# Kernel optimization log

Measured on AMD Instinct MI355X. Metric: run time of the kernel, lower is better.

The kernel has to match this reference:

```python
import jax, jax.numpy as jnp
import numpy as np

N, E, B = 4096, 12288, 64
CLIP, HID, H = 768, 1024, 4
PREFIX, MBART = 4, 768
C2 = PREFIX * MBART
NEG_SLOPE = 0.2


def setup_inputs() -> dict:
    key = jax.random.key(0)
    ks = jax.random.split(key, 30)
    s = 0.05

    def nrm(k, shape, sc=s):
        return jax.random.normal(k, shape, dtype=jnp.float32) * sc

    inp = {
        "x": nrm(ks[0], (N, CLIP), 1.0),
        "edge_index": jax.random.randint(ks[1], (2, E), 0, N),
        "edge_attr": nrm(ks[2], (E, CLIP), 1.0),
        "batch": jnp.sort(jax.random.randint(ks[3], (N,), 0, B)),
        # GATConv 1 (clip_dim -> hidden, H heads, concat=False)
        "W1": nrm(ks[4], (CLIP, H, HID)),
        "att_src1": nrm(ks[5], (H, HID)),
        "att_dst1": nrm(ks[6], (H, HID)),
        "W_edge1": nrm(ks[7], (CLIP, H, HID)),
        "att_edge1": nrm(ks[8], (H, HID)),
        "bias1": jnp.zeros((HID,), jnp.float32),
        "prelu1": jnp.float32(0.25),
        # GATConv 2 (hidden -> prefix*mbart, H heads, concat=False)
        "W2": nrm(ks[9], (HID, H, C2)),
        "att_src2": nrm(ks[10], (H, C2)),
        "att_dst2": nrm(ks[11], (H, C2)),
        "W_edge2": nrm(ks[12], (CLIP, H, C2)),
        "att_edge2": nrm(ks[13], (H, C2)),
        "bias2": jnp.zeros((C2,), jnp.float32),
        "prelu2": jnp.float32(0.25),
        # AttentionalAggregation gate_nn: Linear/PReLU/Linear/PReLU/Linear
        "gW1": nrm(ks[14], (C2, HID)),
        "gb1": jnp.zeros((HID,), jnp.float32),
        "ga1": jnp.float32(0.25),
        "gW2": nrm(ks[15], (HID, HID)),
        "gb2": jnp.zeros((HID,), jnp.float32),
        "ga2": jnp.float32(0.25),
        "gW3": nrm(ks[16], (HID, 1)),
        "gb3": jnp.zeros((1,), jnp.float32),
    }
    return inp


def _prelu(x, a):
    return jnp.where(x >= 0, x, a * x)


def _gat_conv(x, src, dst, edge_attr, W, att_s, att_d, W_e, att_e, bias, n):
    # PyG GATConv, concat=False: shared lin for src/dst, edge-attention term,
    # leaky_relu, segment softmax over destination neighborhoods, scatter-add.
    xl = jnp.einsum('nd,dhc->nhc', x, W)                  # [N,H,C]
    a_s = jnp.einsum('nhc,hc->nh', xl, att_s)             # [N,H]
    a_d = jnp.einsum('nhc,hc->nh', xl, att_d)             # [N,H]
    # fuse lin_edge + att_edge: alpha_e = edge_attr @ (W_e . att_e)
    w_e = jnp.einsum('dhc,hc->dh', W_e, att_e)            # [D_edge,H]
    a_e = edge_attr @ w_e                                 # [E,H]
    alpha = jax.nn.leaky_relu(a_s[src] + a_d[dst] + a_e, NEG_SLOPE)
    # segment softmax grouped by dst
    amax = jax.ops.segment_max(alpha, dst, num_segments=n)
    amax = jnp.where(jnp.isfinite(amax), amax, 0.0)
    ex = jnp.exp(alpha - amax[dst])
    den = jax.ops.segment_sum(ex, dst, num_segments=n)
    coef = ex / (den[dst] + 1e-16)                        # [E,H]
    msg = coef[:, :, None] * xl[src]                      # [E,H,C]
    out = jax.ops.segment_sum(msg, dst, num_segments=n)   # [N,H,C]
    return out.mean(axis=1) + bias                        # concat=False -> head mean


def _forward(x, edge_index, edge_attr, batch,
             W1, att_src1, att_dst1, W_edge1, att_edge1, bias1, prelu1,
             W2, att_src2, att_dst2, W_edge2, att_edge2, bias2, prelu2,
             gW1, gb1, ga1, gW2, gb2, ga2, gW3, gb3):
    n = x.shape[0]
    src, dst = edge_index[0], edge_index[1]
    # add_self_loops with fill_value='mean': self-loop edge_attr = mean of
    # incoming edge_attr per destination node (0 if isolated)
    ones = jnp.ones((src.shape[0],), x.dtype)
    deg = jax.ops.segment_sum(ones, dst, num_segments=n)
    mean_attr = jax.ops.segment_sum(edge_attr, dst, num_segments=n) / jnp.clip(deg, 1.0)[:, None]
    loops = jnp.arange(n)
    src_a = jnp.concatenate([src, loops])
    dst_a = jnp.concatenate([dst, loops])
    ea = jnp.concatenate([edge_attr, mean_attr], axis=0)

    h = _gat_conv(x, src_a, dst_a, ea, W1, att_src1, att_dst1, W_edge1, att_edge1, bias1, n)
    h = _prelu(h, prelu1)
    h = _gat_conv(h, src_a, dst_a, ea, W2, att_src2, att_dst2, W_edge2, att_edge2, bias2, n)
    h = _prelu(h, prelu2)

    # AttentionalAggregation: gate_nn -> segment softmax over batch -> weighted sum
    g = _prelu(h @ gW1 + gb1, ga1)
    g = _prelu(g @ gW2 + gb2, ga2)
    gate = g @ gW3 + gb3                                   # [N,1]
    gmax = jax.ops.segment_max(gate, batch, num_segments=B)
    gmax = jnp.where(jnp.isfinite(gmax), gmax, 0.0)
    eg = jnp.exp(gate - gmax[batch])
    den = jax.ops.segment_sum(eg, batch, num_segments=B)
    coef = eg / (den[batch] + 1e-16)
    pooled = jax.ops.segment_sum(coef * h, batch, num_segments=B)  # [B,C2]
    return pooled.reshape(-1, PREFIX, MBART)


def reference(x, edge_index, edge_attr, batch,
              W1, att_src1, att_dst1, W_edge1, att_edge1, bias1, prelu1,
              W2, att_src2, att_dst2, W_edge2, att_edge2, bias2, prelu2,
              gW1, gb1, ga1, gW2, gb2, ga2, gW3, gb3):
    return _forward(x, edge_index, edge_attr, batch,
                    W1, att_src1, att_dst1, W_edge1, att_edge1, bias1, prelu1,
                    W2, att_src2, att_dst2, W_edge2, att_edge2, bias2, prelu2,
                    gW1, gb1, ga1, gW2, gb2, ga2, gW3, gb3)
```

## Files before the change

### kernel.cpp

```cpp
#include <hip/hip_runtime.h>
#include <stdint.h>
#include <stddef.h>

#define N_NODES  4096
#define N_EDGES  12288
#define EA_EDGES 16384
#define NBATCH   64
#define CLIPD    768
#define HIDD     1024
#define C2D      3072
#define NEG_SLOPE 0.2f
#define MAXDEG   96

typedef unsigned short u16;
typedef short bf16x8 __attribute__((ext_vector_type(8)));
typedef float f32x4  __attribute__((ext_vector_type(4)));

static __device__ __forceinline__ float b2f(u16 u) {
    union { float f; unsigned int i; } v; v.i = ((unsigned int)u) << 16; return v.f;
}
static __device__ __forceinline__ u16 f2b(float f) {
    union { float f; unsigned int i; } v; v.f = f;
    unsigned int r = (v.i + 0x7fffu + ((v.i >> 16) & 1u)) >> 16;
    return (u16)r;
}
static __device__ __forceinline__ void ld4(const float* p, float v[4]) {
    float4 t = *(const float4*)p;
    v[0] = t.x; v[1] = t.y; v[2] = t.z; v[3] = t.w;
}
static __device__ __forceinline__ void ld4(const u16* p, float v[4]) {
    ushort4 t = *(const ushort4*)p;
    v[0] = b2f(t.x); v[1] = b2f(t.y); v[2] = b2f(t.z); v[3] = b2f(t.w);
}

static __device__ __forceinline__ float wsum(float v) {
#pragma unroll
    for (int o = 32; o > 0; o >>= 1) v += __shfl_xor(v, o, 64);
    return v;
}
static __device__ __forceinline__ float wmax(float v) {
#pragma unroll
    for (int o = 32; o > 0; o >>= 1) v = fmaxf(v, __shfl_xor(v, o, 64));
    return v;
}
static __device__ __forceinline__ int lower_bound(const int* a, int n, int key) {
    int lo = 0, hi = n;
    while (lo < hi) { int m = (lo + hi) >> 1; if (a[m] < key) lo = m + 1; else hi = m; }
    return lo;
}

#define GLD16(gp, lp)                                                            \
    __builtin_amdgcn_global_load_lds((const __attribute__((address_space(1))) void*)(gp), \
                                     (__attribute__((address_space(3))) void*)(lp), 16, 0, 0)

__global__ void k_deg(const int* __restrict__ dst, int* __restrict__ deg) {
    int e = blockIdx.x * 256 + threadIdx.x;
    if (e < N_EDGES) atomicAdd(&deg[dst[e]], 1);
}

__global__ void k_scan(const int* __restrict__ deg, int* __restrict__ offs) {
    __shared__ int s[1024];
    int t = threadIdx.x;
    int v[4]; int sum = 0;
#pragma unroll
    for (int i = 0; i < 4; i++) { v[i] = deg[t * 4 + i] + 1; sum += v[i]; }
    s[t] = sum; __syncthreads();
    for (int st = 1; st < 1024; st <<= 1) {
        int x = 0;
        if (t >= st) x = s[t - st];
        __syncthreads();
        s[t] += x;
        __syncthreads();
    }
    int run = s[t] - sum;
#pragma unroll
    for (int i = 0; i < 4; i++) { offs[t * 4 + i] = run; run += v[i]; }
    if (t == 1023) offs[N_NODES] = run;
}

__global__ void k_fill(const int* __restrict__ dst, const int* __restrict__ offs,
                       int* __restrict__ cur, int* __restrict__ csr) {
    int id = blockIdx.x * 256 + threadIdx.x;
    if (id >= EA_EDGES) return;
    int d = (id < N_EDGES) ? dst[id] : (id - N_EDGES);
    int p = atomicAdd(&cur[d], 1);
    csr[offs[d] + p] = id;
}

static __device__ void reduce_w_body(const float* __restrict__ W, const float* __restrict__ attA,
                                     const float* __restrict__ attB, float* __restrict__ out,
                                     int C, int col0, int d) {
    int t = threadIdx.x;
    float acc[8] = {0, 0, 0, 0, 0, 0, 0, 0};
    for (int c = t * 4; c < C; c += 1024) {
#pragma unroll
        for (int h = 0; h < 4; h++) {
            float4 w = *(const float4*)&W[((size_t)d * 4 + h) * C + c];
            float4 a = *(const float4*)&attA[h * C + c];
            acc[h] += w.x * a.x + w.y * a.y + w.z * a.z + w.w * a.w;
            if (attB) {
                float4 bv = *(const float4*)&attB[h * C + c];
                acc[4 + h] += w.x * bv.x + w.y * bv.y + w.z * bv.z + w.w * bv.w;
            }
        }
    }
    __shared__ float red[4][8];
    int lane = t & 63, wv = t >> 6;
#pragma unroll
    for (int j = 0; j < 8; j++) acc[j] = wsum(acc[j]);
    if (lane == 0) {
#pragma unroll
        for (int j = 0; j < 8; j++) red[wv][j] = acc[j];
    }
    __syncthreads();
    if (t < 8) {
        float s = red[0][t] + red[1][t] + red[2][t] + red[3][t];
        if (attB) out[d * 8 + col0 + t] = s;
        else if (t < 4) out[d * 8 + col0 + t] = s;
    }
}

__global__ void k_reduce_all(const float* __restrict__ W1, const float* __restrict__ as1,
                             const float* __restrict__ ad1, float* __restrict__ vsd1,
                             const float* __restrict__ We1, const float* __restrict__ ae1,
                             const float* __restrict__ W2, const float* __restrict__ as2,
                             const float* __restrict__ ad2, float* __restrict__ vsd2,
                             const float* __restrict__ We2, const float* __restrict__ ae2,
                             float* __restrict__ we12) {
    int b = blockIdx.x;
    if (b < CLIPD)                   reduce_w_body(W1, as1, ad1, vsd1, HIDD, 0, b);
    else if (b < 2 * CLIPD)          reduce_w_body(We1, ae1, nullptr, we12, HIDD, 0, b - CLIPD);
    else if (b < 2 * CLIPD + HIDD)   reduce_w_body(W2, as2, ad2, vsd2, C2D, 0, b - 2 * CLIPD);
    else                             reduce_w_body(We2, ae2, nullptr, we12, C2D, 4, b - 2 * CLIPD - HIDD);
}

template <typename T>
static __device__ void gemv8_body(const T* __restrict__ X, int K, const float* __restrict__ Wr,
                                  float* __restrict__ out, int row) {
    int lane = threadIdx.x & 63;
    float acc[8] = {0, 0, 0, 0, 0, 0, 0, 0};
    const T* xp = X + (size_t)row * K;
    for (int k = lane * 4; k < K; k += 256) {
        float xv[4]; ld4(xp + k, xv);
#pragma unroll
        for (int kk = 0; kk < 4; kk++) {
            const float4* w = (const float4*)(Wr + (size_t)(k + kk) * 8);
            float4 w0 = w[0], w1 = w[1];
            acc[0] += xv[kk] * w0.x; acc[1] += xv[kk] * w0.y;
            acc[2] += xv[kk] * w0.z; acc[3] += xv[kk] * w0.w;
            acc[4] += xv[kk] * w1.x; acc[5] += xv[kk] * w1.y;
            acc[6] += xv[kk] * w1.z; acc[7] += xv[kk] * w1.w;
        }
    }
#pragma unroll
    for (int j = 0; j < 8; j++) acc[j] = wsum(acc[j]);
    if (lane == 0) {
#pragma unroll
        for (int j = 0; j < 8; j++) out[(size_t)row * 8 + j] = acc[j];
    }
}

template <typename T>
__global__ void k_gemv8(const T* __restrict__ X, int K, const float* __restrict__ Wr,
                        float* __restrict__ out, int rows) {
    int row = blockIdx.x * 4 + (threadIdx.x >> 6);
    if (row < rows) gemv8_body(X, K, Wr, out, row);
}

__global__ void k_gemv8_dual(const float* __restrict__ Xa, const float* __restrict__ Wa,
                             float* __restrict__ outA, int rowsA,
                             const float* __restrict__ Xb, const float* __restrict__ Wb,
                             float* __restrict__ outB) {
    int row = blockIdx.x * 4 + (threadIdx.x >> 6);
    if (row < rowsA) gemv8_body(Xa, CLIPD, Wa, outA, row);
    else             gemv8_body(Xb, CLIPD, Wb, outB, row - rowsA);
}

__global__ void k_selfloop(float* __restrict__ ae, const int* __restrict__ csr,
                           const int* __restrict__ offs, const int* __restrict__ deg) {
    int n = blockIdx.x * 256 + threadIdx.x;
    if (n >= N_NODES) return;
    float s[8] = {0, 0, 0, 0, 0, 0, 0, 0};
    int lo = offs[n], hi = offs[n + 1];
    for (int i = lo; i < hi; i++) {
        int eid = csr[i];
        if (eid < N_EDGES) {
            const float4* p = (const float4*)(ae + (size_t)eid * 8);
            float4 a = p[0], b = p[1];
            s[0] += a.x; s[1] += a.y; s[2] += a.z; s[3] += a.w;
            s[4] += b.x; s[5] += b.y; s[6] += b.z; s[7] += b.w;
        }
    }
    float inv = 1.0f / (float)(deg[n] > 0 ? deg[n] : 1);
    float4* o = (float4*)(ae + (size_t)(N_EDGES + n) * 8);
    float4 o0, o1;
    o0.x = s[0] * inv; o0.y = s[1] * inv; o0.z = s[2] * inv; o0.w = s[3] * inv;
    o1.x = s[4] * inv; o1.y = s[5] * inv; o1.z = s[6] * inv; o1.w = s[7] * inv;
    o[0] = o0; o[1] = o1;
}

template <typename T>
__global__ void k_attn_agg(const T* __restrict__ feat, int D,
                           const float* __restrict__ asd, const float* __restrict__ ae, int aecol,
                           const int* __restrict__ offs, const int* __restrict__ csr,
                           const int* __restrict__ src, u16* __restrict__ agg) {
    int n = blockIdx.x, t = threadIdx.x;
    __shared__ int sl[MAXDEG];
    __shared__ float cf[MAXDEG][4];
    int lo = offs[n];
    int cnt = offs[n + 1] - lo;
    if (cnt > MAXDEG) cnt = MAXDEG;
    for (int i = t; i < cnt; i += 256) {
        int eid = csr[lo + i];
        int s = (eid < N_EDGES) ? src[eid] : n;
        sl[i] = s;
#pragma unroll
        for (int h = 0; h < 4; h++) {
            float al = asd[(size_t)s * 8 + h] + asd[(size_t)n * 8 + 4 + h] +
                       ae[(size_t)eid * 8 + aecol + h];
            cf[i][h] = (al >= 0.f) ? al : NEG_SLOPE * al;
        }
    }
    __syncthreads();
    {
        int wv = t >> 6, lane = t & 63;
        float mx = -1e30f;
        for (int i = lane; i < cnt; i += 64) mx = fmaxf(mx, cf[i][wv]);
        mx = wmax(mx);
        float ds = 0.f;
        for (int i = lane; i < cnt; i += 64) {
            float e = __expf(cf[i][wv] - mx); cf[i][wv] = e; ds += e;
        }
        ds = wsum(ds);
        float inv = 1.0f / (ds + 1e-16f);
        for (int i = lane; i < cnt; i += 64) cf[i][wv] *= inv;
    }
    __syncthreads();
    for (int d4 = t * 4; d4 < D; d4 += 1024) {
        float a[4][4] = {};
        for (int i = 0; i < cnt; i++) {
            float4 c4 = *(const float4*)cf[i];
            float v[4]; ld4(feat + (size_t)sl[i] * D + d4, v);
#pragma unroll
            for (int dj = 0; dj < 4; dj++) {
                a[dj][0] += c4.x * v[dj]; a[dj][1] += c4.y * v[dj];
                a[dj][2] += c4.z * v[dj]; a[dj][3] += c4.w * v[dj];
            }
        }
        u16* op = agg + (size_t)n * 4 * D + (size_t)d4 * 4;
#pragma unroll
        for (int dj = 0; dj < 4; dj++) {
            ushort4 pk;
            pk.x = f2b(a[dj][0]); pk.y = f2b(a[dj][1]);
            pk.z = f2b(a[dj][2]); pk.w = f2b(a[dj][3]);
            *(ushort4*)(op + dj * 4) = pk;
        }
    }
}

__global__ void k_transpose(const float* __restrict__ in, u16* __restrict__ out, int R, int C) {
    __shared__ float tile[64][65];
    int tx = threadIdx.x, ty = threadIdx.y;
    int rb = blockIdx.y * 64, cb = blockIdx.x * 64;
    for (int i = ty; i < 64; i += 4) tile[i][tx] = in[(size_t)(rb + i) * C + cb + tx];
    __syncthreads();
    int linear = ty * 64 + tx;
#pragma unroll
    for (int jj = 0; jj < 4; jj++) {
        int idx = linear + jj * 256;
        int j = idx >> 4, s4 = (idx & 15) * 4;
        ushort4 pk;
        pk.x = f2b(tile[s4 + 0][j]);
        pk.y = f2b(tile[s4 + 1][j]);
        pk.z = f2b(tile[s4 + 2][j]);
        pk.w = f2b(tile[s4 + 3][j]);
        *(ushort4*)(out + (size_t)(cb + j) * R + rb + s4) = pk;
    }
}

template <int BN, int KSUB>
__global__ __launch_bounds__(256, 2) void k_gemm(
        const u16* __restrict__ A, const u16* __restrict__ Bt, void* __restrict__ Cout,
        const float* __restrict__ bias, const float* __restrict__ prelu, float scale,
        int N, int K, int f32out) {
    constexpr int NJ = BN / 32;
    constexpr int NBCH = BN * 8 / 256;
    __shared__ __align__(16) u16 As[KSUB * 128 * 64];
    __shared__ __align__(16) u16 Bs[KSUB * BN * 64];
    int tid = threadIdx.x;
    int lane = tid & 63, wv = tid >> 6;
    int gx = gridDim.x;
    int bx = blockIdx.x, by = blockIdx.y;
    if ((gx & 7) == 0) {
        int flat = by * gx + bx;
        int nx_per = gx >> 3;
        int xcd = flat & 7, idx = flat >> 3;
        bx = xcd * nx_per + idx % nx_per;
        by = idx / nx_per;
    }
    int m0 = by * 128, n0 = bx * BN;
    const u16* agp[4]; int alo[4];
#pragma unroll
    for (int u = 0; u < 4; u++) {
        int c = tid + u * 256;
        int r = c >> 3, kb = (c & 7) ^ (r & 7);
        agp[u] = A + (size_t)(m0 + r) * K + kb * 8;
        alo[u] = c * 8;
    }
    const u16* bgp[NBCH]; int blo[NBCH];
#pragma unroll
    for (int u = 0; u < NBCH; u++) {
        int c = tid + u * 256;
        int r = c >> 3, kb = (c & 7) ^ (r & 7);
        bgp[u] = Bt + (size_t)(n0 + r) * K + kb * 8;
        blo[u] = c * 8;
    }
    int wm = wv & 1, wn = wv >> 1;
    int rl = lane & 15, q = lane >> 4;
    int swz = rl & 7;
    int mb = wm * 64 + rl;
    int nb = wn * (NJ * 16) + rl;
    f32x4 acc[4][NJ] = {};
    for (int k0 = 0; k0 < K; k0 += 64 * KSUB) {
        __syncthreads();
#pragma unroll
        for (int su = 0; su < KSUB; su++) {
#pragma unroll
            for (int u = 0; u < 4; u++)    GLD16(agp[u] + su * 64, As + su * (128 * 64) + alo[u]);
#pragma unroll
            for (int u = 0; u < NBCH; u++) GLD16(bgp[u] + su * 64, Bs + su * (BN * 64) + blo[u]);
        }
#pragma unroll
        for (int u = 0; u < 4; u++)    agp[u] += 64 * KSUB;
#pragma unroll
        for (int u = 0; u < NBCH; u++) bgp[u] += 64 * KSUB;
        __syncthreads();
#pragma unroll
        for (int su = 0; su < KSUB; su++) {
            const u16* Asb = As + su * (128 * 64);
            const u16* Bsb = Bs + su * (BN * 64);
            bf16x8 af[4][2], bfr[NJ][2];
#pragma unroll
            for (int i = 0; i < 4; i++)
#pragma unroll
                for (int s = 0; s < 2; s++)
                    af[i][s] = *(const bf16x8*)(Asb + (((mb + i * 16) * 8 + ((q + 4 * s) ^ swz)) * 8));
#pragma unroll
            for (int j = 0; j < NJ; j++)
#pragma unroll
                for (int s = 0; s < 2; s++)
                    bfr[j][s] = *(const bf16x8*)(Bsb + (((nb + j * 16) * 8 + ((q + 4 * s) ^ swz)) * 8));
#pragma unroll
            for (int i = 0; i < 4; i++)
#pragma unroll
                for (int j = 0; j < NJ; j++) {
                    acc[i][j] = __builtin_amdgcn_mfma_f32_16x16x32_bf16(af[i][0], bfr[j][0], acc[i][j], 0, 0, 0);
                    acc[i][j] = __builtin_amdgcn_mfma_f32_16x16x32_bf16(af[i][1], bfr[j][1], acc[i][j], 0, 0, 0);
                }
        }
    }
    float pa = prelu[0];
    int r0w = (lane >> 4) * 4;
    int cc = lane & 15;
#pragma unroll
    for (int j = 0; j < NJ; j++) {
        int col = n0 + wn * (NJ * 16) + j * 16 + cc;
        float bv = bias[col];
#pragma unroll
        for (int i = 0; i < 4; i++) {
#pragma unroll
            for (int r = 0; r < 4; r++) {
                int row = m0 + wm * 64 + i * 16 + r0w + r;
                float v = acc[i][j][r] * scale + bv;
                v = (v >= 0.f) ? v : pa * v;
                if (f32out) ((float*)Cout)[(size_t)row * N + col] = v;
                else        ((u16*)Cout)[(size_t)row * N + col] = f2b(v);
            }
        }
    }
}

__global__ void k_gate(const float* __restrict__ g2, const float* __restrict__ gW3,
                       const float* __restrict__ gb3, float* __restrict__ gate) {
    int wv = threadIdx.x >> 6, lane = threadIdx.x & 63;
    int n = blockIdx.x * 4 + wv;
    if (n >= N_NODES) return;
    float s = 0.f;
    const float* gp = g2 + (size_t)n * HIDD;
    for (int k = lane * 4; k < HIDD; k += 256) {
        float4 a = *(const float4*)(gp + k);
        float4 w = *(const float4*)(gW3 + k);
        s += a.x * w.x + a.y * w.y + a.z * w.z + a.w * w.w;
    }
    s = wsum(s);
    if (lane == 0) gate[n] = s + gb3[0];
}

__global__ void k_pool(const float* __restrict__ gate, const u16* __restrict__ h2,
                       const int* __restrict__ batch, float* __restrict__ out) {
    int b = blockIdx.x, t = threadIdx.x;
    int c = blockIdx.y * 1024 + t * 4;
    int lo = lower_bound(batch, N_NODES, b);
    int hi = lower_bound(batch, N_NODES, b + 1);
    int cnt = hi - lo;
    if (cnt <= 0) {
        float4 z; z.x = z.y = z.z = z.w = 0.f;
        *(float4*)(out + (size_t)b * C2D + c) = z;
        return;
    }
    if (cnt > 256) cnt = 256;
    __shared__ float w[256];
    __shared__ float red[4];
    int lane = t & 63, wv = t >> 6;
    float mx = -1e30f;
    for (int i = t; i < cnt; i += 256) mx = fmaxf(mx, gate[lo + i]);
    mx = wmax(mx);
    if (lane == 0) red[wv] = mx;
    __syncthreads();
    mx = fmaxf(fmaxf(red[0], red[1]), fmaxf(red[2], red[3]));
    __syncthreads();
    float ds = 0.f;
    for (int i = t; i < cnt; i += 256) { float e = __expf(gate[lo + i] - mx); w[i] = e; ds += e; }
    ds = wsum(ds);
    if (lane == 0) red[wv] = ds;
    __syncthreads();
    float inv = 1.0f / (red[0] + red[1] + red[2] + red[3] + 1e-16f);
    float4 acc; acc.x = acc.y = acc.z = acc.w = 0.f;
    const u16* hp = h2 + (size_t)lo * C2D + c;
    for (int i = 0; i < cnt; i++) {
        ushort4 hv = *(const ushort4*)hp; hp += C2D;
        float wi = w[i];
        acc.x += wi * b2f(hv.x); acc.y += wi * b2f(hv.y);
        acc.z += wi * b2f(hv.z); acc.w += wi * b2f(hv.w);
    }
    acc.x *= inv; acc.y *= inv; acc.z *= inv; acc.w *= inv;
    *(float4*)(out + (size_t)b * C2D + c) = acc;
}

extern "C" void kernel_launch(void* const* d_in, const int* in_sizes, int n_in,
                              void* d_out, int out_size, void* d_ws, size_t ws_size,
                              hipStream_t stream) {
    (void)in_sizes; (void)n_in; (void)out_size; (void)ws_size;
    const float* x      = (const float*)d_in[0];
    const int*   eidx   = (const int*)d_in[1];
    const float* eattr  = (const float*)d_in[2];
    const int*   batch  = (const int*)d_in[3];
    const float* W1     = (const float*)d_in[4];
    const float* att_s1 = (const float*)d_in[5];
    const float* att_d1 = (const float*)d_in[6];
    const float* We1    = (const float*)d_in[7];
    const float* att_e1 = (const float*)d_in[8];
    const float* bias1  = (const float*)d_in[9];
    const float* prelu1 = (const float*)d_in[10];
    const float* W2     = (const float*)d_in[11];
    const float* att_s2 = (const float*)d_in[12];
    const float* att_d2 = (const float*)d_in[13];
    const float* We2    = (const float*)d_in[14];
    const float* att_e2 = (const float*)d_in[15];
    const float* bias2  = (const float*)d_in[16];
    const float* prelu2 = (const float*)d_in[17];
    const float* gW1    = (const float*)d_in[18];
    const float* gb1    = (const float*)d_in[19];
    const float* ga1    = (const float*)d_in[20];
    const float* gW2    = (const float*)d_in[21];
    const float* gb2    = (const float*)d_in[22];
    const float* ga2    = (const float*)d_in[23];
    const float* gW3    = (const float*)d_in[24];
    const float* gb3    = (const float*)d_in[25];
    const int* srcA = eidx;
    const int* dstA = eidx + N_EDGES;

    char* wp = (char*)d_ws;
    auto alloc = [&](size_t bytes) -> void* {
        void* p = (void*)wp; wp += (bytes + 255) & ~(size_t)255; return p;
    };
    int*   deg  = (int*)alloc(N_NODES * 4);
    int*   cur  = (int*)alloc(N_NODES * 4);
    int*   offs = (int*)alloc((N_NODES + 1) * 4);
    int*   csr  = (int*)alloc(EA_EDGES * 4);
    float* vsd1 = (float*)alloc(CLIPD * 8 * 4);
    float* we12 = (float*)alloc(CLIPD * 8 * 4);
    float* vsd2 = (float*)alloc(HIDD * 8 * 4);
    float* ae   = (float*)alloc((size_t)EA_EDGES * 8 * 4);
    float* asd1 = (float*)alloc((size_t)N_NODES * 8 * 4);
    float* asd2 = (float*)alloc((size_t)N_NODES * 8 * 4);
    float* gate = (float*)alloc(N_NODES * 4);
    char*  aggU = (char*)alloc((size_t)N_NODES * 4096 * 2);
    u16*   agg1 = (u16*)aggU;
    u16*   agg2 = (u16*)aggU;
    float* g2   = (float*)aggU;
    u16*   h1   = (u16*)alloc((size_t)N_NODES * HIDD * 2);
    u16*   g1   = h1;
    u16*   h2   = (u16*)alloc((size_t)N_NODES * C2D * 2);
    u16*   Btb  = (u16*)alloc((size_t)C2D * 4096 * 2);

    hipMemsetAsync(deg, 0, N_NODES * 4, stream);
    hipMemsetAsync(cur, 0, N_NODES * 4, stream);

    k_deg<<<(N_EDGES + 255) / 256, 256, 0, stream>>>(dstA, deg);
    k_scan<<<1, 1024, 0, stream>>>(deg, offs);
    k_fill<<<(EA_EDGES + 255) / 256, 256, 0, stream>>>(dstA, offs, cur, csr);

    k_reduce_all<<<2 * CLIPD + HIDD + CLIPD, 256, 0, stream>>>(
        W1, att_s1, att_d1, vsd1, We1, att_e1, W2, att_s2, att_d2, vsd2, We2, att_e2, we12);

    k_gemv8_dual<<<(N_EDGES + N_NODES) / 4, 256, 0, stream>>>(
        eattr, we12, ae, N_EDGES, x, vsd1, asd1);
    k_selfloop<<<(N_NODES + 255) / 256, 256, 0, stream>>>(ae, csr, offs, deg);

    k_attn_agg<float><<<N_NODES, 256, 0, stream>>>(x, CLIPD, asd1, ae, 0, offs, csr, srcA, agg1);
    k_transpose<<<dim3(HIDD / 64, C2D / 64), dim3(64, 4), 0, stream>>>(W1, Btb, C2D, HIDD);
    k_gemm<64, 2><<<dim3(HIDD / 64, N_NODES / 128), 256, 0, stream>>>(
        agg1, Btb, h1, bias1, prelu1, 0.25f, HIDD, C2D, 0);

    k_gemv8<u16><<<N_NODES / 4, 256, 0, stream>>>(h1, HIDD, vsd2, asd2, N_NODES);
    k_attn_agg<u16><<<N_NODES, 256, 0, stream>>>(h1, HIDD, asd2, ae, 4, offs, csr, srcA, agg2);
    k_transpose<<<dim3(C2D / 64, 4096 / 64), dim3(64, 4), 0, stream>>>(W2, Btb, 4096, C2D);
    k_gemm<128, 1><<<dim3(C2D / 128, N_NODES / 128), 256, 0, stream>>>(
        agg2, Btb, h2, bias2, prelu2, 0.25f, C2D, 4096, 0);

    k_transpose<<<dim3(HIDD / 64, C2D / 64), dim3(64, 4), 0, stream>>>(gW1, Btb, C2D, HIDD);
    k_gemm<64, 2><<<dim3(HIDD / 64, N_NODES / 128), 256, 0, stream>>>(
        h2, Btb, g1, gb1, ga1, 1.0f, HIDD, C2D, 0);
    k_transpose<<<dim3(HIDD / 64, HIDD / 64), dim3(64, 4), 0, stream>>>(gW2, Btb, HIDD, HIDD);
    k_gemm<64, 2><<<dim3(HIDD / 64, N_NODES / 128), 256, 0, stream>>>(
        g1, Btb, (void*)g2, gb2, ga2, 1.0f, HIDD, HIDD, 1);
    k_gate<<<N_NODES / 4, 256, 0, stream>>>(g2, gW3, gb3, gate);

    k_pool<<<dim3(NBATCH, 3), 256, 0, stream>>>(gate, h2, batch, (float*)d_out);
}
```

Measured before the change: 557.0 us.

## Fuse gate projection into final GEMM, batch weight transposes, inline self-loop attention

Folds the final gate linear (gW3) into the epilogue of the last gate-MLP GEMM using shuffle reductions and atomicAdd into a zeroed gate buffer. This removes the fp32 g2 intermediate and the separate gate kernel. All four weight transposes are batched into a single launch with separate destination buffers when workspace allows. The self-loop edge-attention mean is computed inside the attention-aggregation kernel instead of a separate pass. Atomic gate accumulation adds nondeterministic summation order, the gb3 bias is dropped as softmax-invariant, and more workspace is used.

```diff
diff --git a/kernel.cpp b/kernel.cpp
--- a/kernel.cpp
+++ b/kernel.cpp
@@ -176,29 +176,6 @@
     else             gemv8_body(Xb, CLIPD, Wb, outB, row - rowsA);
 }
 
-__global__ void k_selfloop(float* __restrict__ ae, const int* __restrict__ csr,
-                           const int* __restrict__ offs, const int* __restrict__ deg) {
-    int n = blockIdx.x * 256 + threadIdx.x;
-    if (n >= N_NODES) return;
-    float s[8] = {0, 0, 0, 0, 0, 0, 0, 0};
-    int lo = offs[n], hi = offs[n + 1];
-    for (int i = lo; i < hi; i++) {
-        int eid = csr[i];
-        if (eid < N_EDGES) {
-            const float4* p = (const float4*)(ae + (size_t)eid * 8);
-            float4 a = p[0], b = p[1];
-            s[0] += a.x; s[1] += a.y; s[2] += a.z; s[3] += a.w;
-            s[4] += b.x; s[5] += b.y; s[6] += b.z; s[7] += b.w;
-        }
-    }
-    float inv = 1.0f / (float)(deg[n] > 0 ? deg[n] : 1);
-    float4* o = (float4*)(ae + (size_t)(N_EDGES + n) * 8);
-    float4 o0, o1;
-    o0.x = s[0] * inv; o0.y = s[1] * inv; o0.z = s[2] * inv; o0.w = s[3] * inv;
-    o1.x = s[4] * inv; o1.y = s[5] * inv; o1.z = s[6] * inv; o1.w = s[7] * inv;
-    o[0] = o0; o[1] = o1;
-}
-
 template <typename T>
 __global__ void k_attn_agg(const T* __restrict__ feat, int D,
                            const float* __restrict__ asd, const float* __restrict__ ae, int aecol,
@@ -207,23 +184,41 @@
     int n = blockIdx.x, t = threadIdx.x;
     __shared__ int sl[MAXDEG];
     __shared__ float cf[MAXDEG][4];
+    __shared__ float er[MAXDEG][4];
+    __shared__ int sidx;
+    if (t == 0) sidx = -1;
     int lo = offs[n];
     int cnt = offs[n + 1] - lo;
     if (cnt > MAXDEG) cnt = MAXDEG;
+    __syncthreads();
     for (int i = t; i < cnt; i += 256) {
         int eid = csr[lo + i];
-        int s = (eid < N_EDGES) ? src[eid] : n;
+        bool slf = (eid >= N_EDGES);
+        int s = slf ? n : src[eid];
         sl[i] = s;
+        if (slf) sidx = i;
 #pragma unroll
         for (int h = 0; h < 4; h++) {
-            float al = asd[(size_t)s * 8 + h] + asd[(size_t)n * 8 + 4 + h] +
-                       ae[(size_t)eid * 8 + aecol + h];
+            float aev = slf ? 0.f : ae[(size_t)eid * 8 + aecol + h];
+            er[i][h] = aev;
+            float al = asd[(size_t)s * 8 + h] + asd[(size_t)n * 8 + 4 + h] + aev;
             cf[i][h] = (al >= 0.f) ? al : NEG_SLOPE * al;
         }
     }
     __syncthreads();
+    int wv = t >> 6, lane = t & 63;
     {
-        int wv = t >> 6, lane = t & 63;
+        float se = 0.f;
+        for (int i = lane; i < cnt; i += 64) se += er[i][wv];
+        se = wsum(se);
+        if (lane == 0 && sidx >= 0) {
+            float al = asd[(size_t)n * 8 + wv] + asd[(size_t)n * 8 + 4 + wv] +
+                       se / (float)(cnt > 1 ? cnt - 1 : 1);
+            cf[sidx][wv] = (al >= 0.f) ? al : NEG_SLOPE * al;
+        }
+    }
+    __syncthreads();
+    {
         float mx = -1e30f;
         for (int i = lane; i < cnt; i += 64) mx = fmaxf(mx, cf[i][wv]);
         mx = wmax(mx);
@@ -258,10 +253,11 @@
     }
 }
 
-__global__ void k_transpose(const float* __restrict__ in, u16* __restrict__ out, int R, int C) {
+static __device__ void transpose_body(const float* __restrict__ in, u16* __restrict__ out,
+                                      int R, int C, int bx, int by) {
     __shared__ float tile[64][65];
     int tx = threadIdx.x, ty = threadIdx.y;
-    int rb = blockIdx.y * 64, cb = blockIdx.x * 64;
+    int rb = by * 64, cb = bx * 64;
     for (int i = ty; i < 64; i += 4) tile[i][tx] = in[(size_t)(rb + i) * C + cb + tx];
     __syncthreads();
     int linear = ty * 64 + tx;
@@ -278,11 +274,29 @@
     }
 }
 
-template <int BN, int KSUB>
+__global__ void k_transpose(const float* __restrict__ in, u16* __restrict__ out, int R, int C) {
+    transpose_body(in, out, R, C, blockIdx.x, blockIdx.y);
+}
+
+__global__ void k_transpose_all(const float* __restrict__ W1, u16* __restrict__ W1t,
+                                const float* __restrict__ W2, u16* __restrict__ W2t,
+                                const float* __restrict__ gW1, u16* __restrict__ gW1t,
+                                const float* __restrict__ gW2, u16* __restrict__ gW2t) {
+    int b = blockIdx.x;
+    const float* in; u16* out; int R, C, lb, txc;
+    if (b < 768)       { in = W1;  out = W1t;  R = 3072; C = 1024; lb = b;        txc = 16; }
+    else if (b < 3840) { in = W2;  out = W2t;  R = 4096; C = 3072; lb = b - 768;  txc = 48; }
+    else if (b < 4608) { in = gW1; out = gW1t; R = 3072; C = 1024; lb = b - 3840; txc = 16; }
+    else               { in = gW2; out = gW2t; R = 1024; C = 1024; lb = b - 4608; txc = 16; }
+    transpose_body(in, out, R, C, lb % txc, lb / txc);
+}
+
+template <int BN, int KSUB, int GATE>
 __global__ __launch_bounds__(256, 2) void k_gemm(
         const u16* __restrict__ A, const u16* __restrict__ Bt, void* __restrict__ Cout,
         const float* __restrict__ bias, const float* __restrict__ prelu, float scale,
-        int N, int K, int f32out) {
+        int N, int K, int f32out,
+        const float* __restrict__ gW3, float* __restrict__ gateOut) {
     constexpr int NJ = BN / 32;
     constexpr int NBCH = BN * 8 / 256;
     __shared__ __align__(16) u16 As[KSUB * 128 * 64];
@@ -362,6 +376,35 @@
     float pa = prelu[0];
     int r0w = (lane >> 4) * 4;
     int cc = lane & 15;
+    if (GATE) {
+        float w3[NJ], bvj[NJ];
+#pragma unroll
+        for (int j = 0; j < NJ; j++) {
+            int col = n0 + wn * (NJ * 16) + j * 16 + cc;
+            w3[j] = gW3[col];
+            bvj[j] = bias[col];
+        }
+#pragma unroll
+        for (int i = 0; i < 4; i++) {
+#pragma unroll
+            for (int r = 0; r < 4; r++) {
+                float p = 0.f;
+#pragma unroll
+                for (int j = 0; j < NJ; j++) {
+                    float v = acc[i][j][r] * scale + bvj[j];
+                    v = (v >= 0.f) ? v : pa * v;
+                    p += v * w3[j];
+                }
+                p += __shfl_xor(p, 1, 64); p += __shfl_xor(p, 2, 64);
+                p += __shfl_xor(p, 4, 64); p += __shfl_xor(p, 8, 64);
+                if (cc == 0) {
+                    int row = m0 + wm * 64 + i * 16 + r0w + r;
+                    atomicAdd(&gateOut[row], p);
+                }
+            }
+        }
+        return;
+    }
 #pragma unroll
     for (int j = 0; j < NJ; j++) {
         int col = n0 + wn * (NJ * 16) + j * 16 + cc;
@@ -378,22 +421,6 @@
             }
         }
     }
-}
-
-__global__ void k_gate(const float* __restrict__ g2, const float* __restrict__ gW3,
-                       const float* __restrict__ gb3, float* __restrict__ gate) {
-    int wv = threadIdx.x >> 6, lane = threadIdx.x & 63;
-    int n = blockIdx.x * 4 + wv;
-    if (n >= N_NODES) return;
-    float s = 0.f;
-    const float* gp = g2 + (size_t)n * HIDD;
-    for (int k = lane * 4; k < HIDD; k += 256) {
-        float4 a = *(const float4*)(gp + k);
-        float4 w = *(const float4*)(gW3 + k);
-        s += a.x * w.x + a.y * w.y + a.z * w.z + a.w * w.w;
-    }
-    s = wsum(s);
-    if (lane == 0) gate[n] = s + gb3[0];
 }
 
 __global__ void k_pool(const float* __restrict__ gate, const u16* __restrict__ h2,
@@ -440,7 +467,7 @@
 extern "C" void kernel_launch(void* const* d_in, const int* in_sizes, int n_in,
                               void* d_out, int out_size, void* d_ws, size_t ws_size,
                               hipStream_t stream) {
-    (void)in_sizes; (void)n_in; (void)out_size; (void)ws_size;
+    (void)in_sizes; (void)n_in; (void)out_size;
     const float* x      = (const float*)d_in[0];
     const int*   eidx   = (const int*)d_in[1];
     const float* eattr  = (const float*)d_in[2];
@@ -466,7 +493,6 @@
     const float* gb2    = (const float*)d_in[22];
     const float* ga2    = (const float*)d_in[23];
     const float* gW3    = (const float*)d_in[24];
-    const float* gb3    = (const float*)d_in[25];
     const int* srcA = eidx;
     const int* dstA = eidx + N_EDGES;
 
@@ -481,21 +507,32 @@
     float* vsd1 = (float*)alloc(CLIPD * 8 * 4);
     float* we12 = (float*)alloc(CLIPD * 8 * 4);
     float* vsd2 = (float*)alloc(HIDD * 8 * 4);
-    float* ae   = (float*)alloc((size_t)EA_EDGES * 8 * 4);
+    float* ae   = (float*)alloc((size_t)N_EDGES * 8 * 4);
     float* asd1 = (float*)alloc((size_t)N_NODES * 8 * 4);
     float* asd2 = (float*)alloc((size_t)N_NODES * 8 * 4);
     float* gate = (float*)alloc(N_NODES * 4);
     char*  aggU = (char*)alloc((size_t)N_NODES * 4096 * 2);
     u16*   agg1 = (u16*)aggU;
     u16*   agg2 = (u16*)aggU;
-    float* g2   = (float*)aggU;
     u16*   h1   = (u16*)alloc((size_t)N_NODES * HIDD * 2);
     u16*   g1   = h1;
     u16*   h2   = (u16*)alloc((size_t)N_NODES * C2D * 2);
-    u16*   Btb  = (u16*)alloc((size_t)C2D * 4096 * 2);
+    size_t used = (size_t)(wp - (char*)d_ws);
+    bool fused_tr = (ws_size == 0) || (ws_size > used + (size_t)42 * 1024 * 1024);
+    u16 *W1t, *W2t, *gW1t, *gW2t;
+    if (fused_tr) {
+        W1t  = (u16*)alloc((size_t)1024 * 3072 * 2);
+        W2t  = (u16*)alloc((size_t)3072 * 4096 * 2);
+        gW1t = (u16*)alloc((size_t)1024 * 3072 * 2);
+        gW2t = (u16*)alloc((size_t)1024 * 1024 * 2);
+    } else {
+        u16* Btb = (u16*)alloc((size_t)C2D * 4096 * 2);
+        W1t = W2t = gW1t = gW2t = Btb;
+    }
 
     hipMemsetAsync(deg, 0, N_NODES * 4, stream);
     hipMemsetAsync(cur, 0, N_NODES * 4, stream);
+    hipMemsetAsync(gate, 0, N_NODES * 4, stream);
 
     k_deg<<<(N_EDGES + 255) / 256, 256, 0, stream>>>(dstA, deg);
     k_scan<<<1, 1024, 0, stream>>>(deg, offs);
@@ -503,29 +540,33 @@
 
     k_reduce_all<<<2 * CLIPD + HIDD + CLIPD, 256, 0, stream>>>(
         W1, att_s1, att_d1, vsd1, We1, att_e1, W2, att_s2, att_d2, vsd2, We2, att_e2, we12);
+    if (fused_tr)
+        k_transpose_all<<<4864, dim3(64, 4), 0, stream>>>(W1, W1t, W2, W2t, gW1, gW1t, gW2, gW2t);
 
     k_gemv8_dual<<<(N_EDGES + N_NODES) / 4, 256, 0, stream>>>(
         eattr, we12, ae, N_EDGES, x, vsd1, asd1);
-    k_selfloop<<<(N_NODES + 255) / 256, 256, 0, stream>>>(ae, csr, offs, deg);
 
     k_attn_agg<float><<<N_NODES, 256, 0, stream>>>(x, CLIPD, asd1, ae, 0, offs, csr, srcA, agg1);
-    k_transpose<<<dim3(HIDD / 64, C2D / 64), dim3(64, 4), 0, stream>>>(W1, Btb, C2D, HIDD);
-    k_gemm<64, 2><<<dim3(HIDD / 64, N_NODES / 128), 256, 0, stream>>>(
-        agg1, Btb, h1, bias1, prelu1, 0.25f, HIDD, C2D, 0);
+    if (!fused_tr)
+        k_transpose<<<dim3(HIDD / 64, C2D / 64), dim3(64, 4), 0, stream>>>(W1, W1t, C2D, HIDD);
+    k_gemm<64, 2, 0><<<dim3(HIDD / 64, N_NODES / 128), 256, 0, stream>>>(
+        agg1, W1t, h1, bias1, prelu1, 0.25f, HIDD, C2D, 0, nullptr, nullptr);
 
     k_gemv8<u16><<<N_NODES / 4, 256, 0, stream>>>(h1, HIDD, vsd2, asd2, N_NODES);
     k_attn_agg<u16><<<N_NODES, 256, 0, stream>>>(h1, HIDD, asd2, ae, 4, offs, csr, srcA, agg2);
-    k_transpose<<<dim3(C2D / 64, 4096 / 64), dim3(64, 4), 0, stream>>>(W2, Btb, 4096, C2D);
-    k_gemm<128, 1><<<dim3(C2D / 128, N_NODES / 128), 256, 0, stream>>>(
-        agg2, Btb, h2, bias2, prelu2, 0.25f, C2D, 4096, 0);
-
-    k_transpose<<<dim3(HIDD / 64, C2D / 64), dim3(64, 4), 0, stream>>>(gW1, Btb, C2D, HIDD);
-    k_gemm<64, 2><<<dim3(HIDD / 64, N_NODES / 128), 256, 0, stream>>>(
-        h2, Btb, g1, gb1, ga1, 1.0f, HIDD, C2D, 0);
-    k_transpose<<<dim3(HIDD / 64, HIDD / 64), dim3(64, 4), 0, stream>>>(gW2, Btb, HIDD, HIDD);
-    k_gemm<64, 2><<<dim3(HIDD / 64, N_NODES / 128), 256, 0, stream>>>(
-        g1, Btb, (void*)g2, gb2, ga2, 1.0f, HIDD, HIDD, 1);
-    k_gate<<<N_NODES / 4, 256, 0, stream>>>(g2, gW3, gb3, gate);
+    if (!fused_tr)
+        k_transpose<<<dim3(C2D / 64, 4096 / 64), dim3(64, 4), 0, stream>>>(W2, W2t, 4096, C2D);
+    k_gemm<128, 1, 0><<<dim3(C2D / 128, N_NODES / 128), 256, 0, stream>>>(
+        agg2, W2t, h2, bias2, prelu2, 0.25f, C2D, 4096, 0, nullptr, nullptr);
+
+    if (!fused_tr)
+        k_transpose<<<dim3(HIDD / 64, C2D / 64), dim3(64, 4), 0, stream>>>(gW1, gW1t, C2D, HIDD);
+    k_gemm<64, 2, 0><<<dim3(HIDD / 64, N_NODES / 128), 256, 0, stream>>>(
+        h2, gW1t, g1, gb1, ga1, 1.0f, HIDD, C2D, 0, nullptr, nullptr);
+    if (!fused_tr)
+        k_transpose<<<dim3(HIDD / 64, HIDD / 64), dim3(64, 4), 0, stream>>>(gW2, gW2t, HIDD, HIDD);
+    k_gemm<64, 2, 1><<<dim3(HIDD / 64, N_NODES / 128), 256, 0, stream>>>(
+        g1, gW2t, nullptr, gb2, ga2, 1.0f, HIDD, HIDD, 0, gW3, gate);
 
     k_pool<<<dim3(NBATCH, 3), 256, 0, stream>>>(gate, h2, batch, (float*)d_out);
 }
```

Measured after the change: 555.3 us. Within noise of the previous version (-0.3%).
